# Optimization experiments

Hardware: AMD Instinct MI355X
Metric: run time of the kernel (lower is better)

## Reference

```python
import jax, jax.numpy as jnp
import numpy as np


def setup_inputs() -> dict:
    key = jax.random.key(0)
    k1, k2 = jax.random.split(key)
    pred = jax.random.normal(k1, (8, 4096, 2), dtype=jnp.float32)
    target = jax.random.normal(k2, (8, 4096, 2), dtype=jnp.float32)
    return {"pred": pred, "target": target}


def reference(pred, target):
    # pred: [B, N, D], target: [B, M, D]
    # pairwise euclidean distances per batch: [B, N, M]
    diff = pred[:, :, None, :] - target[:, None, :, :]  # [B, N, M, D]
    dist = jnp.sqrt(jnp.sum(diff * diff, axis=-1))       # [B, N, M]
    # directed Hausdorff h(a,b) = max_i min_j d(a_i, b_j)
    h_ab = jnp.max(jnp.min(dist, axis=2), axis=1)        # [B]
    h_ba = jnp.max(jnp.min(dist, axis=1), axis=1)        # [B]
    score = jnp.maximum(h_ab, h_ba)                      # symmetric Hausdorff per batch
    return jnp.mean(score)
```

## Files before the change

### kernel.cpp

```cpp
#include <hip/hip_runtime.h>
#include <hip/hip_bf16.h>
#include <math.h>


#define B 8
#define N 4096
#define TPB 256
#define IB 4
#define JC 16
#define JTILE (N / JC)

__global__ __launch_bounds__(TPB) void hk_partial(const float* __restrict__ pred,
                                                  const float* __restrict__ target,
                                                  float* __restrict__ pw,
                                                  float* __restrict__ out) {
    const int bx  = blockIdx.x;
    const int ib  = bx & 3;
    const int jc  = bx >> 2;
    const int b   = blockIdx.y;
    const int dir = blockIdx.z;

    if (bx == 0 && b == 0 && dir == 0 && threadIdx.x == 0) out[0] = 0.f;

    const float2* P = reinterpret_cast<const float2*>(dir == 0 ? pred : target) + (size_t)b * N;
    const float2* Q = reinterpret_cast<const float2*>(dir == 0 ? target : pred) + (size_t)b * N;

    __shared__ float4 sQ[JTILE];
    {
        const int t = threadIdx.x;
        float2 q = Q[jc * JTILE + t];
        sQ[t] = make_float4(q.x, q.y, fmaf(q.x, q.x, q.y * q.y), 0.f);
    }
    __syncthreads();

    float m2x[IB], m2y[IB], pp[IB], mn[IB];
    const int i0 = ib * (TPB * IB) + threadIdx.x;
    #pragma unroll
    for (int k = 0; k < IB; ++k) {
        float2 p = P[i0 + k * TPB];
        m2x[k] = -2.f * p.x;
        m2y[k] = -2.f * p.y;
        pp[k]  = fmaf(p.x, p.x, p.y * p.y);
        mn[k]  = 3.402823466e38f;
    }

    #pragma unroll 4
    for (int j = 0; j < JTILE; ++j) {
        float4 q = sQ[j];
        #pragma unroll
        for (int k = 0; k < IB; ++k) {
            float t1 = fmaf(m2y[k], q.y, q.z);
            t1 = fmaf(m2x[k], q.x, t1);
            mn[k] = fminf(mn[k], t1);
        }
    }

    float* dst = pw + (size_t)(((dir * B + b) * JC + jc)) * N;
    #pragma unroll
    for (int k = 0; k < IB; ++k)
        dst[i0 + k * TPB] = mn[k] + pp[k];
}

__global__ __launch_bounds__(TPB) void hk_reduce(const float* __restrict__ pw,
                                                 float* __restrict__ out) {
    const int b = blockIdx.x;
    const int t = threadIdx.x;

    __shared__ float sred[TPB / 64];
    float h2[2];

    for (int dir = 0; dir < 2; ++dir) {
        float mx = -3.402823466e38f;
        for (int i = t; i < N; i += TPB) {
            const float* base = pw + (size_t)((dir * B + b) * JC) * N + i;
            float mnv = base[0];
            #pragma unroll
            for (int jc = 1; jc < JC; ++jc) mnv = fminf(mnv, base[(size_t)jc * N]);
            mx = fmaxf(mx, mnv);
        }
        #pragma unroll
        for (int off = 32; off > 0; off >>= 1)
            mx = fmaxf(mx, __shfl_down(mx, off, 64));
        if ((t & 63) == 0) sred[t >> 6] = mx;
        __syncthreads();
        if (t == 0) {
            float bm = sred[0];
            #pragma unroll
            for (int w = 1; w < TPB / 64; ++w) bm = fmaxf(bm, sred[w]);
            h2[dir] = bm;
        }
        __syncthreads();
    }

    if (t == 0) {
        float s = sqrtf(fmaxf(fmaxf(h2[0], h2[1]), 0.f));
        atomicAdd(out, s * 0.125f);
    }
}

extern "C" void kernel_launch(void* const* d_in, const int* in_sizes, int n_in,
                              void* d_out, int out_size, void* d_ws, size_t ws_size,
                              hipStream_t stream) {
    const float* pred   = (const float*)d_in[0];
    const float* target = (const float*)d_in[1];
    float* out = (float*)d_out;
    float* pw  = (float*)d_ws;

    dim3 grid(64, B, 2);
    hk_partial<<<grid, TPB, 0, stream>>>(pred, target, pw, out);
    hk_reduce<<<B, TPB, 0, stream>>>(pw, out);
}
```

Before: 86.68 us.

## Split reduction across many blocks and add final kernel; pair-unroll min loop

```diff
diff --git a/kernel.cpp b/kernel.cpp
--- a/kernel.cpp
+++ b/kernel.cpp
@@ -9,18 +9,16 @@
 #define IB 4
 #define JC 16
 #define JTILE (N / JC)
+#define ITILES (N / TPB)
 
 __global__ __launch_bounds__(TPB) void hk_partial(const float* __restrict__ pred,
                                                   const float* __restrict__ target,
-                                                  float* __restrict__ pw,
-                                                  float* __restrict__ out) {
+                                                  float* __restrict__ pw) {
     const int bx  = blockIdx.x;
     const int ib  = bx & 3;
     const int jc  = bx >> 2;
     const int b   = blockIdx.y;
     const int dir = blockIdx.z;
-
-    if (bx == 0 && b == 0 && dir == 0 && threadIdx.x == 0) out[0] = 0.f;
 
     const float2* P = reinterpret_cast<const float2*>(dir == 0 ? pred : target) + (size_t)b * N;
     const float2* Q = reinterpret_cast<const float2*>(dir == 0 ? target : pred) + (size_t)b * N;
@@ -44,57 +42,69 @@
         mn[k]  = 3.402823466e38f;
     }
 
-    #pragma unroll 4
-    for (int j = 0; j < JTILE; ++j) {
-        float4 q = sQ[j];
+    #pragma unroll 2
+    for (int j = 0; j < JTILE; j += 2) {
+        float4 qa = sQ[j];
+        float4 qb = sQ[j + 1];
         #pragma unroll
         for (int k = 0; k < IB; ++k) {
-            float t1 = fmaf(m2y[k], q.y, q.z);
-            t1 = fmaf(m2x[k], q.x, t1);
-            mn[k] = fminf(mn[k], t1);
+            float ta = fmaf(m2x[k], qa.x, fmaf(m2y[k], qa.y, qa.z));
+            float tb = fmaf(m2x[k], qb.x, fmaf(m2y[k], qb.y, qb.z));
+            mn[k] = fminf(mn[k], fminf(ta, tb));
         }
     }
 
-    float* dst = pw + (size_t)(((dir * B + b) * JC + jc)) * N;
+    float* dst = pw + (size_t)((dir * B + b) * JC + jc) * N;
     #pragma unroll
     for (int k = 0; k < IB; ++k)
         dst[i0 + k * TPB] = mn[k] + pp[k];
 }
 
-__global__ __launch_bounds__(TPB) void hk_reduce(const float* __restrict__ pw,
-                                                 float* __restrict__ out) {
-    const int b = blockIdx.x;
-    const int t = threadIdx.x;
+__global__ __launch_bounds__(TPB) void hk_maxred(const float* __restrict__ pw,
+                                                 float* __restrict__ pw2) {
+    const int tile = blockIdx.x;
+    const int b    = blockIdx.y;
+    const int dir  = blockIdx.z;
+    const int t    = threadIdx.x;
+
+    const float* base = pw + (size_t)((dir * B + b) * JC) * N + tile * TPB + t;
+    float mnv = base[0];
+    #pragma unroll
+    for (int jc = 1; jc < JC; ++jc) mnv = fminf(mnv, base[(size_t)jc * N]);
+
+    float mx = mnv;
+    #pragma unroll
+    for (int off = 32; off > 0; off >>= 1)
+        mx = fmaxf(mx, __shfl_down(mx, off, 64));
 
     __shared__ float sred[TPB / 64];
-    float h2[2];
+    if ((t & 63) == 0) sred[t >> 6] = mx;
+    __syncthreads();
+    if (t == 0) {
+        float bm = sred[0];
+        #pragma unroll
+        for (int w = 1; w < TPB / 64; ++w) bm = fmaxf(bm, sred[w]);
+        pw2[(dir * B + b) * ITILES + tile] = bm;
+    }
+}
 
-    for (int dir = 0; dir < 2; ++dir) {
-        float mx = -3.402823466e38f;
-        for (int i = t; i < N; i += TPB) {
-            const float* base = pw + (size_t)((dir * B + b) * JC) * N + i;
-            float mnv = base[0];
-            #pragma unroll
-            for (int jc = 1; jc < JC; ++jc) mnv = fminf(mnv, base[(size_t)jc * N]);
-            mx = fmaxf(mx, mnv);
-        }
+__global__ __launch_bounds__(64) void hk_final(const float* __restrict__ pw2,
+                                               float* __restrict__ out) {
+    const int t = threadIdx.x;
+    __shared__ float h2[2 * B];
+    if (t < 2 * B) {
+        float mx = pw2[t * ITILES];
         #pragma unroll
-        for (int off = 32; off > 0; off >>= 1)
-            mx = fmaxf(mx, __shfl_down(mx, off, 64));
-        if ((t & 63) == 0) sred[t >> 6] = mx;
-        __syncthreads();
-        if (t == 0) {
-            float bm = sred[0];
-            #pragma unroll
-            for (int w = 1; w < TPB / 64; ++w) bm = fmaxf(bm, sred[w]);
-            h2[dir] = bm;
-        }
-        __syncthreads();
+        for (int k = 1; k < ITILES; ++k) mx = fmaxf(mx, pw2[t * ITILES + k]);
+        h2[t] = mx;
     }
-
+    __syncthreads();
     if (t == 0) {
-        float s = sqrtf(fmaxf(fmaxf(h2[0], h2[1]), 0.f));
-        atomicAdd(out, s * 0.125f);
+        float s = 0.f;
+        #pragma unroll
+        for (int b = 0; b < B; ++b)
+            s += sqrtf(fmaxf(fmaxf(h2[b], h2[B + b]), 0.f));
+        out[0] = s * (1.0f / B);
     }
 }
 
@@ -105,8 +115,11 @@
     const float* target = (const float*)d_in[1];
     float* out = (float*)d_out;
     float* pw  = (float*)d_ws;
+    float* pw2 = (float*)((char*)d_ws + (size_t)2 * B * JC * N * sizeof(float));
 
-    dim3 grid(64, B, 2);
-    hk_partial<<<grid, TPB, 0, stream>>>(pred, target, pw, out);
-    hk_reduce<<<B, TPB, 0, stream>>>(pw, out);
+    dim3 g1(64, B, 2);
+    hk_partial<<<g1, TPB, 0, stream>>>(pred, target, pw);
+    dim3 g2(ITILES, B, 2);
+    hk_maxred<<<g2, TPB, 0, stream>>>(pw, pw2);
+    hk_final<<<1, 64, 0, stream>>>(pw2, out);
 }
```

Result: faster. 77.46 us (-10.6%).
